# Performance work log

Hardware: AMD Instinct MI355X
Metric: run time of the kernel (lower is better)

Reference implementation:

```python
import jax, jax.numpy as jnp
import numpy as np
from jax import lax

B, T, F, C = 2, 249, 64, 256   # fixed by alpha/beta weight shapes in build()
K = 3                          # conv kernel size
FILT = 256                     # q/k conv filters (both blocks)
V = 256                        # v conv filters (both blocks)
OUT_CH = 64                    # conv2d_final filters (hardcoded)


def conv2d(x, w, b):
    # NHWC 'same' conv, stride 1, dilation 1
    return lax.conv_general_dilated(
        x, w, window_strides=(1, 1), padding='SAME',
        dimension_numbers=('NHWC', 'HWIO', 'NHWC')) + b


def attn_block(x, wq, bq, wk, bk, wv, bv):
    # x: [B, H, L, C]; attention over L per (batch, H) slice
    q = conv2d(x, wq, bq)          # [B,H,L,FILT]
    k = conv2d(x, wk, bk)          # [B,H,L,FILT]
    v = conv2d(x, wv, bv)          # [B,H,L,V]
    scores = jnp.einsum('bhqc,bhkc->bhqk', q, k)   # [B,H,L,L]
    dist = jax.nn.softmax(scores, axis=-1)
    return jnp.einsum('bhqk,bhkc->bhqc', dist, v)  # [B,H,L,V]


def setup_inputs() -> dict:
    key = jax.random.key(0)
    ks = jax.random.split(key, 18)
    s = 0.05
    d = {'x': jax.random.normal(ks[0], (B, T, F, C), jnp.float32)}
    names = ['wq_f', 'wk_f', 'wv_f', 'wq_t', 'wk_t', 'wv_t']
    outs = [FILT, FILT, V, FILT, FILT, V]
    for i, (n, o) in enumerate(zip(names, outs)):
        d[n] = jax.random.normal(ks[1 + i], (K, K, C, o), jnp.float32) * s
        d['b' + n[1:]] = jnp.zeros((o,), jnp.float32)
    d['w_final'] = jax.random.normal(ks[8], (K, K, V + V + C, OUT_CH), jnp.float32) * s
    d['b_final'] = jnp.zeros((OUT_CH,), jnp.float32)
    d['alpha'] = jax.random.uniform(ks[9], (B, T, F, V), jnp.float32, -0.05, 0.05)
    d['beta'] = jax.random.uniform(ks[10], (B, T, F, V), jnp.float32, -0.05, 0.05)
    return d


def reference(x, wq_f, bq_f, wk_f, bk_f, wv_f, bv_f,
              wq_t, bq_t, wk_t, bk_t, wv_t, bv_t,
              w_final, b_final, alpha, beta):
    # AFAB: transpose to [B,F,T,C], attend over time axis T
    xt = jnp.transpose(x, (0, 2, 1, 3))
    out_freq = attn_block(xt, wq_f, bq_f, wk_f, bk_f, wv_f, bv_f)
    out_freq = jnp.transpose(out_freq, (0, 2, 1, 3))  # back to [B,T,F,V]
    # ATAB: attend over frequency axis F directly on [B,T,F,C]
    out_time = attn_block(x, wq_t, bq_t, wk_t, bk_t, wv_t, bv_t)
    # learned elementwise gating + concat + final conv (concatenation=True path)
    fused = jnp.concatenate([alpha * out_freq, beta * out_time, x], axis=-1)
    return conv2d(fused, w_final, b_final)
```

## Files before the change

### kernel.cpp

```cpp
#include <hip/hip_runtime.h>


typedef _Float16 f16;
typedef _Float16 f16x8 __attribute__((ext_vector_type(8)));
typedef float    f32x4 __attribute__((ext_vector_type(4)));

#define B_   2
#define T_   249
#define F_   64
#define TP   251
#define FP   66
#define PIXB (T_*F_)
#define NPIX (B_*PIXB)
#define LPAD 256
#define XPOS (B_*TP*FP)

static constexpr size_t FUSED_BYTES = (size_t)B_*TP*FP*768*2;
static constexpr size_t XPAD_BYTES  = (size_t)B_*TP*FP*256*2;
static constexpr size_t QF_BYTES    = (size_t)B_*64*LPAD*256*2;
static constexpr size_t QT_BYTES    = (size_t)B_*T_*64*256*2;
static constexpr size_t WT_BYTES    = (size_t)9*1536*256*2;
static constexpr size_t WFT_BYTES   = (size_t)9*64*768*2;

static constexpr size_t OFF_FUSED = 0;
static constexpr size_t OFF_XPAD  = OFF_FUSED + FUSED_BYTES;
static constexpr size_t OFF_QF    = OFF_XPAD  + XPAD_BYTES;
static constexpr size_t OFF_KF    = OFF_QF + QF_BYTES;
static constexpr size_t OFF_VF    = OFF_KF + QF_BYTES;
static constexpr size_t OFF_QT    = OFF_VF + QF_BYTES;
static constexpr size_t OFF_KT    = OFF_QT + QT_BYTES;
static constexpr size_t OFF_VT    = OFF_KT + QT_BYTES;
static constexpr size_t OFF_WT    = OFF_VT + QT_BYTES;
static constexpr size_t OFF_WFT   = OFF_WT + WT_BYTES;
static constexpr size_t OFF_BALL  = OFF_WFT + WFT_BYTES;
static constexpr size_t OFF_BF    = OFF_BALL + 1536*4;
static constexpr size_t WS_NEED   = OFF_BF + 64*4;

__device__ __forceinline__ f32x4 mfma16(f16x8 a, f16x8 b, f32x4 c) {
    return __builtin_amdgcn_mfma_f32_16x16x32_f16(a, b, c, 0, 0, 0);
}

__device__ __forceinline__ void gl_lds16(const void* g, void* l) {
    __builtin_amdgcn_global_load_lds(
        (const __attribute__((address_space(1))) unsigned int*)(unsigned long long)g,
        (__attribute__((address_space(3))) unsigned int*)(unsigned int)(unsigned long long)l,
        16, 0, 0);
}

__global__ __launch_bounds__(256) void prep_w(
    const float* __restrict__ wqf, const float* __restrict__ wkf, const float* __restrict__ wvf,
    const float* __restrict__ wqt, const float* __restrict__ wkt, const float* __restrict__ wvt,
    const float* __restrict__ wfin,
    const float* __restrict__ bqf, const float* __restrict__ bkf, const float* __restrict__ bvf,
    const float* __restrict__ bqt, const float* __restrict__ bkt, const float* __restrict__ bvt,
    const float* __restrict__ bfin,
    f16* __restrict__ wT, f16* __restrict__ wfT,
    float* __restrict__ biasAll, float* __restrict__ biasF)
{
    int idx = blockIdx.x*256 + threadIdx.x;
    if (idx < 9*1536*256) {
        int tap = idx / (1536*256);
        int r   = idx - tap*(1536*256);
        int n = r >> 8, c = r & 255;
        int dt = tap/3 - 1, df = tap%3 - 1;
        int blk = n >> 8, nl = n & 255;
        const float* w; int kh, kw;
        if (blk < 3) { w = (blk==0) ? wqf : (blk==1) ? wkf : wvf; kh = df+1; kw = dt+1; }
        else         { w = (blk==3) ? wqt : (blk==4) ? wkt : wvt; kh = dt+1; kw = df+1; }
        wT[idx] = (f16)w[((kh*3 + kw)*256 + c)*256 + nl];
    }
    if (idx < 9*64*768) {
        int tap = idx / (64*768);
        int r   = idx - tap*(64*768);
        int oc = r / 768, cin = r - oc*768;
        int dt = tap/3 - 1, df = tap%3 - 1;
        wfT[idx] = (f16)wfin[(((dt+1)*3 + (df+1))*768 + cin)*64 + oc];
    }
    if (idx < 1536) {
        int blk = idx >> 8, nl = idx & 255;
        const float* bb = (blk==0)?bqf:(blk==1)?bkf:(blk==2)?bvf:(blk==3)?bqt:(blk==4)?bkt:bvt;
        biasAll[idx] = bb[nl];
    }
    if (idx < 64) biasF[idx] = bfin[idx];
}

__global__ __launch_bounds__(256) void prep_x(
    const float* __restrict__ x, f16* __restrict__ xpad, f16* __restrict__ fused)
{
    int tid = blockIdx.x*256 + threadIdx.x;
    int pix = tid >> 5, c8 = (tid & 31)*8;
    int b = pix / PIXB; int r = pix - b*PIXB;
    int t = r >> 6, f = r & 63;
    const float* src = x + (size_t)pix*256 + c8;
    f16x8 v;
#pragma unroll
    for (int j = 0; j < 8; ++j) v[j] = (f16)src[j];
    size_t pp = (size_t)(b*TP + t + 1)*FP + (f + 1);
    *(f16x8*)(xpad + pp*256 + c8) = v;
    *(f16x8*)(fused + pp*768 + 512 + c8) = v;
}

__global__ __launch_bounds__(256) void border_zero(
    f16* __restrict__ xpad, f16* __restrict__ fused)
{
    int pix = blockIdx.x*2 + (threadIdx.x >> 7);
    int tl = threadIdx.x & 127;
    int b = pix / 630; int i = pix - b*630;
    int tp, fp;
    if (i < 66)       { tp = 0;   fp = i; }
    else if (i < 132) { tp = 250; fp = i - 66; }
    else { int j = i - 132; tp = 1 + (j >> 1); fp = (j & 1) * 65; }
    size_t pp = (size_t)(b*TP + tp)*FP + fp;
    f16x8 z = {0, 0, 0, 0, 0, 0, 0, 0};
    if (tl < 32) *(f16x8*)(xpad + pp*256 + tl*8) = z;
    if (tl < 96) *(f16x8*)(fused + pp*768 + tl*8) = z;
}

__global__ __launch_bounds__(512, 2) void conv_qkv(
    const f16* __restrict__ xpad, const f16* __restrict__ wT,
    const float* __restrict__ biasAll,
    f16* __restrict__ qf, f16* __restrict__ kf, f16* __restrict__ vf,
    f16* __restrict__ qt, f16* __restrict__ kt_, f16* __restrict__ vt)
{
    __shared__ f16 smemH[448*64];
    __shared__ f16 smemB[2][256*64];

    const int xcd = blockIdx.x & 7, lin = blockIdx.x >> 3;
    const int mtcnt = (xcd < 6) ? 16 : 15;
    if (lin >= 6*mtcnt) return;
    const int mtbase = (xcd < 6) ? xcd*16 : 96 + (xcd - 6)*15;
    const int nt = lin / mtcnt;
    const int mt = mtbase + (lin - nt*mtcnt);

    const int bb_ = mt / 63;
    const int t0  = (mt - bb_*63) * 4;
    const int Gs66 = (bb_*TP + t0) * 66;

    const int l   = threadIdx.x & 63;
    const int wid = threadIdx.x >> 6;
    const int wm = wid >> 2, wn = wid & 3;

    int hOff[7];
#pragma unroll
    for (int j = 0; j < 7; ++j) {
        int pos = j*64 + wid*8 + (l >> 3);
        int ps = pos;
        if (ps > 395) ps = 395;
        { int pm = XPOS - 1 - (bb_*TP + t0)*66; if (ps > pm) ps = pm; }
        int ch = (l & 7) ^ (ps & 7);
        hOff[j] = (Gs66 + ps)*256 + ch*8;
    }
    int bSrc[4];
#pragma unroll
    for (int j = 0; j < 4; ++j) {
        int row = j*64 + wid*8 + (l >> 3);
        int ch = (l & 7) ^ (row & 7);
        bSrc[j] = (nt*256 + row)*256 + ch*8;
    }

    int pos00[8];
#pragma unroll
    for (int m = 0; m < 8; ++m) {
        int r = wm*128 + m*16 + (l & 15);
        pos00[m] = ((r >> 6) + 1)*66 + (r & 63) + 1;
    }
    int bRow[4], bSw[4];
#pragma unroll
    for (int n = 0; n < 4; ++n) {
        int row = wn*64 + n*16 + (l & 15);
        bRow[n] = row*64; bSw[n] = row & 7;
    }

    f32x4 acc[8][4];
#pragma unroll
    for (int m = 0; m < 8; ++m)
#pragma unroll
        for (int n = 0; n < 4; ++n) acc[m][n] = {0.f, 0.f, 0.f, 0.f};

#define HSTAGE(C) do {                                                         \
        _Pragma("unroll")                                                      \
        for (int j_ = 0; j_ < 7; ++j_)                                         \
            gl_lds16(xpad + hOff[j_] + (C)*64,                                 \
                     smemH + (j_*512 + wid*64)*8);                             \
    } while (0)

#define BSTAGE(TAP, C, NB) do {                                                \
        const f16* wt_ = wT + (size_t)(TAP)*(1536*256) + (C)*64;               \
        _Pragma("unroll")                                                      \
        for (int j_ = 0; j_ < 4; ++j_)                                         \
            gl_lds16(wt_ + bSrc[j_], &smemB[NB][(j_*512 + wid*64)*8]);         \
    } while (0)

#define QCOMP(NB, TAPOFF) do {                                                 \
        int pos_[8];                                                           \
        _Pragma("unroll")                                                      \
        for (int m = 0; m < 8; ++m) pos_[m] = pos00[m] + (TAPOFF);             \
        _Pragma("unroll")                                                      \
        for (int kk = 0; kk < 2; ++kk) {                                       \
            const int cch = kk*4 + (l >> 4);                                   \
            f16x8 af[8], bf[4];                                                \
            _Pragma("unroll")                                                  \
            for (int m = 0; m < 8; ++m)                                        \
                af[m] = *(const f16x8*)(smemH + pos_[m]*64 + ((cch ^ (pos_[m] & 7)) << 3)); \
            _Pragma("unroll")                                                  \
            for (int n = 0; n < 4; ++n)                                        \
                bf[n] = *(const f16x8*)(&smemB[NB][0] + bRow[n] + ((cch ^ bSw[n]) << 3)); \
            __builtin_amdgcn_s_setprio(1);                                     \
            _Pragma("unroll")                                                  \
            for (int m = 0; m < 8; ++m)                                        \
                _Pragma("unroll")                                              \
                for (int n = 0; n < 4; ++n)                                    \
                    acc[m][n] = mfma16(af[m], bf[n], acc[m][n]);               \
            __builtin_amdgcn_s_setprio(0);                                     \
        }                                                                      \
    } while (0)

    int buf = 0;
    HSTAGE(0);
    BSTAGE(0, 0, 0);
    __syncthreads();
    for (int c = 0; c < 4; ++c) {
        for (int tap = 0; tap < 9; ++tap) {
            if (tap < 8)      BSTAGE(tap + 1, c, buf ^ 1);
            else if (c < 3)   BSTAGE(0, c + 1, buf ^ 1);
            const int dt = tap/3 - 1, df = tap - (tap/3)*3 - 1;
            QCOMP(buf, dt*66 + df);
            __syncthreads();
            buf ^= 1;
        }
        if (c < 3) {
            HSTAGE(c + 1);
            __syncthreads();
        }
    }
#undef HSTAGE
#undef BSTAGE
#undef QCOMP

    f16* dst = (nt==0)?qf:(nt==1)?kf:(nt==2)?vf:(nt==3)?qt:(nt==4)?kt_:vt;
#pragma unroll
    for (int m = 0; m < 8; ++m) {
#pragma unroll
        for (int rg = 0; rg < 4; ++rg) {
            int row = wm*128 + m*16 + (l >> 4)*4 + rg;
            int t = t0 + (row >> 6), f = row & 63;
            if (t <= 248) {
#pragma unroll
                for (int n = 0; n < 4; ++n) {
                    int col = wn*64 + n*16 + (l & 15);
                    float v = acc[m][n][rg] + biasAll[nt*256 + col];
                    int off;
                    if (nt < 2)       off = ((bb_*64 + f)*LPAD + t)*256 + col;
                    else if (nt == 2) off = ((bb_*64 + f)*256 + col)*LPAD + t;
                    else if (nt < 5)  off = ((bb_*T_ + t)*64 + f)*256 + col;
                    else              off = ((bb_*T_ + t)*256 + col)*64 + f;
                    dst[off] = (f16)v;
                }
            }
        }
    }
}

__global__ __launch_bounds__(256) void attn_f(
    const f16* __restrict__ qf, const f16* __restrict__ kf, const f16* __restrict__ vf,
    const float* __restrict__ alpha, f16* __restrict__ fused)
{
    __shared__ f16 plds[4][16*256];
    const int l = threadIdx.x & 63;
    const int wid = threadIdx.x >> 6;
    const int head = blockIdx.x >> 2;
    const int qb = blockIdx.x & 3;
    const int b = head >> 6, f = head & 63;
    const f16* qh = qf + (size_t)head*LPAD*256;
    const f16* kh = kf + (size_t)head*LPAD*256;
    const f16* vh = vf + (size_t)head*256*LPAD;
    const int qr0 = qb*64 + wid*16;
    f16* pw = &plds[wid][0];

    f16x8 qa[8];
#pragma unroll
    for (int ks = 0; ks < 8; ++ks)
        qa[ks] = *(const f16x8*)(qh + (qr0 + (l & 15))*256 + ks*32 + (l >> 4)*8);

    f32x4 s[16];
#pragma unroll
    for (int nf = 0; nf < 16; ++nf) s[nf] = {0.f, 0.f, 0.f, 0.f};
#pragma unroll
    for (int ks = 0; ks < 8; ++ks)
#pragma unroll
        for (int nf = 0; nf < 16; ++nf) {
            f16x8 bf = *(const f16x8*)(kh + (nf*16 + (l & 15))*256 + ks*32 + (l >> 4)*8);
            s[nf] = mfma16(qa[ks], bf, s[nf]);
        }

    float inv[4];
#pragma unroll
    for (int rg = 0; rg < 4; ++rg) {
        float m = -1e30f;
#pragma unroll
        for (int nf = 0; nf < 16; ++nf)
            if (nf*16 + (l & 15) < T_) m = fmaxf(m, s[nf][rg]);
#pragma unroll
        for (int d = 1; d < 16; d <<= 1) m = fmaxf(m, __shfl_xor(m, d, 64));
        float sum = 0.f;
#pragma unroll
        for (int nf = 0; nf < 16; ++nf) {
            float p = (nf*16 + (l & 15) < T_) ? __expf(s[nf][rg] - m) : 0.f;
            s[nf][rg] = p;
            sum += p;
        }
#pragma unroll
        for (int d = 1; d < 16; d <<= 1) sum += __shfl_xor(sum, d, 64);
        inv[rg] = 1.f / sum;
    }

#pragma unroll
    for (int nf = 0; nf < 16; ++nf)
#pragma unroll
        for (int rg = 0; rg < 4; ++rg) {
            int row = (l >> 4)*4 + rg;
            int col = nf*16 + (l & 15);
            int byte = (row*512 + col*2) ^ ((row & 7) << 4);
            *(f16*)((char*)pw + byte) = (f16)s[nf][rg];
        }

    f32x4 o[16];
#pragma unroll
    for (int nf = 0; nf < 16; ++nf) o[nf] = {0.f, 0.f, 0.f, 0.f};
#pragma unroll
    for (int ks = 0; ks < 8; ++ks) {
        int row = l & 15;
        int cch = ks*4 + (l >> 4);
        int byte = row*512 + ((cch ^ (row & 7)) << 4);
        f16x8 pa = *(const f16x8*)((const char*)pw + byte);
#pragma unroll
        for (int nf = 0; nf < 16; ++nf) {
            f16x8 bf = *(const f16x8*)(vh + (nf*16 + (l & 15))*LPAD + ks*32 + (l >> 4)*8);
            o[nf] = mfma16(pa, bf, o[nf]);
        }
    }

#pragma unroll
    for (int rg = 0; rg < 4; ++rg) {
        int t = qr0 + (l >> 4)*4 + rg;
        if (t < T_) {
#pragma unroll
            for (int nf = 0; nf < 16; ++nf) {
                int c = nf*16 + (l & 15);
                float v = o[nf][rg] * inv[rg] * alpha[((size_t)(b*T_ + t)*64 + f)*256 + c];
                fused[((size_t)(b*TP + t + 1)*FP + (f + 1))*768 + c] = (f16)v;
            }
        }
    }
}

__global__ __launch_bounds__(256) void attn_t(
    const f16* __restrict__ qt, const f16* __restrict__ kt, const f16* __restrict__ vt,
    const float* __restrict__ beta, f16* __restrict__ fused)
{
    __shared__ f16 plds[4][16*64];
    const int l = threadIdx.x & 63;
    const int wid = threadIdx.x >> 6;
    const int head = blockIdx.x;
    const int b = head / T_, t = head - b*T_;
    const f16* qh = qt + (size_t)head*64*256;
    const f16* kh = kt + (size_t)head*64*256;
    const f16* vh = vt + (size_t)head*256*64;
    const int qr0 = wid*16;
    f16* pw = &plds[wid][0];

    f16x8 qa[8];
#pragma unroll
    for (int ks = 0; ks < 8; ++ks)
        qa[ks] = *(const f16x8*)(qh + (qr0 + (l & 15))*256 + ks*32 + (l >> 4)*8);

    f32x4 s[4];
#pragma unroll
    for (int nf = 0; nf < 4; ++nf) s[nf] = {0.f, 0.f, 0.f, 0.f};
#pragma unroll
    for (int ks = 0; ks < 8; ++ks)
#pragma unroll
        for (int nf = 0; nf < 4; ++nf) {
            f16x8 bf = *(const f16x8*)(kh + (nf*16 + (l & 15))*256 + ks*32 + (l >> 4)*8);
            s[nf] = mfma16(qa[ks], bf, s[nf]);
        }

    float inv[4];
#pragma unroll
    for (int rg = 0; rg < 4; ++rg) {
        float m = -1e30f;
#pragma unroll
        for (int nf = 0; nf < 4; ++nf) m = fmaxf(m, s[nf][rg]);
#pragma unroll
        for (int d = 1; d < 16; d <<= 1) m = fmaxf(m, __shfl_xor(m, d, 64));
        float sum = 0.f;
#pragma unroll
        for (int nf = 0; nf < 4; ++nf) {
            float p = __expf(s[nf][rg] - m);
            s[nf][rg] = p;
            sum += p;
        }
#pragma unroll
        for (int d = 1; d < 16; d <<= 1) sum += __shfl_xor(sum, d, 64);
        inv[rg] = 1.f / sum;
    }

#pragma unroll
    for (int nf = 0; nf < 4; ++nf)
#pragma unroll
        for (int rg = 0; rg < 4; ++rg) {
            int row = (l >> 4)*4 + rg;
            int col = nf*16 + (l & 15);
            int byte = (row*128 + col*2) ^ ((row & 7) << 4);
            *(f16*)((char*)pw + byte) = (f16)s[nf][rg];
        }

    f32x4 o[16];
#pragma unroll
    for (int nf = 0; nf < 16; ++nf) o[nf] = {0.f, 0.f, 0.f, 0.f};
#pragma unroll
    for (int ks = 0; ks < 2; ++ks) {
        int row = l & 15;
        int cch = ks*4 + (l >> 4);
        int byte = row*128 + ((cch ^ (row & 7)) << 4);
        f16x8 pa = *(const f16x8*)((const char*)pw + byte);
#pragma unroll
        for (int nf = 0; nf < 16; ++nf) {
            f16x8 bf = *(const f16x8*)(vh + (nf*16 + (l & 15))*64 + ks*32 + (l >> 4)*8);
            o[nf] = mfma16(pa, bf, o[nf]);
        }
    }

#pragma unroll
    for (int rg = 0; rg < 4; ++rg) {
        int fo = qr0 + (l >> 4)*4 + rg;
#pragma unroll
        for (int nf = 0; nf < 16; ++nf) {
            int c = nf*16 + (l & 15);
            float v = o[nf][rg] * inv[rg] * beta[((size_t)(b*T_ + t)*64 + fo)*256 + c];
            fused[((size_t)(b*TP + t + 1)*FP + (fo + 1))*768 + 256 + c] = (f16)v;
        }
    }
}

__global__ __launch_bounds__(256, 2) void conv_final(
    const f16* __restrict__ fused, const f16* __restrict__ wfT,
    const float* __restrict__ biasF, float* __restrict__ out)
{
    __shared__ f16 smemH[288*64];
    __shared__ f16 smemB[2][64*64];

    const int mt = blockIdx.x;
    const int bb = mt / 125;
    const int t0 = (mt - bb*125) * 2;
    const int Gs66 = (bb*TP + t0) * 66;

    const int tid = threadIdx.x;
    const int l   = tid & 63;
    const int wid = tid >> 6;
    const int wm = wid >> 1, wn = wid & 1;

    int hOff[9];
#pragma unroll
    for (int j = 0; j < 9; ++j) {
        int ps = j*32 + (tid >> 3);
        if (ps > 263) ps = 263;
        { int pm = XPOS - 1 - (bb*TP + t0)*66; if (ps > pm) ps = pm; }
        int ch = (tid & 7) ^ (ps & 7);
        hOff[j] = (Gs66 + ps)*768 + ch*8;
    }
    int bSrc[2];
#pragma unroll
    for (int j = 0; j < 2; ++j) {
        int row = j*32 + (tid >> 3);
        int ch  = (tid & 7) ^ (row & 7);
        bSrc[j] = row*768 + ch*8;
    }

    int pos00[4];
#pragma unroll
    for (int m = 0; m < 4; ++m) {
        int r = wm*64 + m*16 + (l & 15);
        pos00[m] = ((r >> 6) + 1)*66 + (r & 63) + 1;
    }
    int bRow[2], bSw[2];
#pragma unroll
    for (int n = 0; n < 2; ++n) {
        int row = wn*32 + n*16 + (l & 15);
        bRow[n] = row*64; bSw[n] = row & 7;
    }

    f32x4 acc[4][2];
#pragma unroll
    for (int m = 0; m < 4; ++m)
#pragma unroll
        for (int n = 0; n < 2; ++n) acc[m][n] = {0.f, 0.f, 0.f, 0.f};

#define FHSTAGE(C) do {                                                        \
        _Pragma("unroll")                                                      \
        for (int j_ = 0; j_ < 9; ++j_)                                         \
            gl_lds16(fused + hOff[j_] + (C)*64,                                \
                     smemH + (j_*256 + wid*64)*8);                             \
    } while (0)

#define FBSTAGE(TAP, C, NB) do {                                               \
        const f16* wt_ = wfT + (size_t)(TAP)*(64*768) + (C)*64;                \
        _Pragma("unroll")                                                      \
        for (int j_ = 0; j_ < 2; ++j_)                                         \
            gl_lds16(wt_ + bSrc[j_], &smemB[NB][(j_*256 + wid*64)*8]);         \
    } while (0)

#define FCOMP(NB, TAPOFF) do {                                                 \
        int pos_[4];                                                           \
        _Pragma("unroll")                                                      \
        for (int m = 0; m < 4; ++m) pos_[m] = pos00[m] + (TAPOFF);             \
        _Pragma("unroll")                                                      \
        for (int kk = 0; kk < 2; ++kk) {                                       \
            const int cch = kk*4 + (l >> 4);                                   \
            f16x8 af[4], bf[2];                                                \
            _Pragma("unroll")                                                  \
            for (int m = 0; m < 4; ++m)                                        \
                af[m] = *(const f16x8*)(smemH + pos_[m]*64 + ((cch ^ (pos_[m] & 7)) << 3)); \
            _Pragma("unroll")                                                  \
            for (int n = 0; n < 2; ++n)                                        \
                bf[n] = *(const f16x8*)(&smemB[NB][0] + bRow[n] + ((cch ^ bSw[n]) << 3)); \
            __builtin_amdgcn_s_setprio(1);                                     \
            _Pragma("unroll")                                                  \
            for (int m = 0; m < 4; ++m)                                        \
                _Pragma("unroll")                                              \
                for (int n = 0; n < 2; ++n)                                    \
                    acc[m][n] = mfma16(af[m], bf[n], acc[m][n]);               \
            __builtin_amdgcn_s_setprio(0);                                     \
        }                                                                      \
    } while (0)

    int buf = 0;
    FHSTAGE(0);
    FBSTAGE(0, 0, 0);
    __syncthreads();
    for (int c = 0; c < 12; ++c) {
        for (int tap = 0; tap < 9; ++tap) {
            if (tap < 8)       FBSTAGE(tap + 1, c, buf ^ 1);
            else if (c < 11)   FBSTAGE(0, c + 1, buf ^ 1);
            const int dt = tap/3 - 1, df = tap - (tap/3)*3 - 1;
            FCOMP(buf, dt*66 + df);
            __syncthreads();
            buf ^= 1;
        }
        if (c < 11) {
            FHSTAGE(c + 1);
            __syncthreads();
        }
    }
#undef FHSTAGE
#undef FBSTAGE
#undef FCOMP

#pragma unroll
    for (int m = 0; m < 4; ++m) {
#pragma unroll
        for (int rg = 0; rg < 4; ++rg) {
            int r = wm*64 + m*16 + (l >> 4)*4 + rg;
            int t = t0 + (r >> 6), f = r & 63;
            if (t <= 248) {
                size_t pix = (size_t)bb*PIXB + t*64 + f;
#pragma unroll
                for (int n = 0; n < 2; ++n) {
                    int oc = wn*32 + n*16 + (l & 15);
                    out[pix*64 + oc] = acc[m][n][rg] + biasF[oc];
                }
            }
        }
    }
}

extern "C" void kernel_launch(void* const* d_in, const int* in_sizes, int n_in,
                              void* d_out, int out_size, void* d_ws, size_t ws_size,
                              hipStream_t stream) {
    (void)in_sizes; (void)n_in; (void)out_size;
    const float* x    = (const float*)d_in[0];
    const float* wqf  = (const float*)d_in[1];
    const float* bqf  = (const float*)d_in[2];
    const float* wkf  = (const float*)d_in[3];
    const float* bkf  = (const float*)d_in[4];
    const float* wvf  = (const float*)d_in[5];
    const float* bvf  = (const float*)d_in[6];
    const float* wqt  = (const float*)d_in[7];
    const float* bqt  = (const float*)d_in[8];
    const float* wkt  = (const float*)d_in[9];
    const float* bkt  = (const float*)d_in[10];
    const float* wvt  = (const float*)d_in[11];
    const float* bvt  = (const float*)d_in[12];
    const float* wfin = (const float*)d_in[13];
    const float* bfin = (const float*)d_in[14];
    const float* alpha= (const float*)d_in[15];
    const float* beta = (const float*)d_in[16];

    if (ws_size < WS_NEED) return;

    char* ws = (char*)d_ws;
    f16* fused  = (f16*)(ws + OFF_FUSED);
    f16* xpad   = (f16*)(ws + OFF_XPAD);
    f16* qf     = (f16*)(ws + OFF_QF);
    f16* kf     = (f16*)(ws + OFF_KF);
    f16* vf     = (f16*)(ws + OFF_VF);
    f16* qt     = (f16*)(ws + OFF_QT);
    f16* kt     = (f16*)(ws + OFF_KT);
    f16* vt     = (f16*)(ws + OFF_VT);
    f16* wT     = (f16*)(ws + OFF_WT);
    f16* wfT    = (f16*)(ws + OFF_WFT);
    float* bAll = (float*)(ws + OFF_BALL);
    float* bF   = (float*)(ws + OFF_BF);

    hipMemsetAsync(vf, 0, QF_BYTES, stream);

    border_zero<<<dim3(630), dim3(256), 0, stream>>>(xpad, fused);
    prep_w<<<dim3((9*1536*256 + 255)/256), dim3(256), 0, stream>>>(
        wqf, wkf, wvf, wqt, wkt, wvt, wfin,
        bqf, bkf, bvf, bqt, bkt, bvt, bfin, wT, wfT, bAll, bF);
    prep_x<<<dim3(NPIX*32/256), dim3(256), 0, stream>>>(x, xpad, fused);
    conv_qkv<<<dim3(768), dim3(512), 0, stream>>>(xpad, wT, bAll, qf, kf, vf, qt, kt, vt);
    attn_f<<<dim3(512), dim3(256), 0, stream>>>(qf, kf, vf, alpha, fused);
    attn_t<<<dim3(498), dim3(256), 0, stream>>>(qt, kt, vt, beta, fused);
    conv_final<<<dim3(250), dim3(256), 0, stream>>>(fused, wfT, bF, (float*)d_out);
}
```

Measured before the change: 502.2 us.

## Restructure QKV conv into 192-row tiles with triple-buffered A and interleaved loads

The implicit-GEMM QKV conv changes from 256-pixel M-tiles (4 time rows, with a halo tile staged once per channel chunk) to 192-pixel tiles of 3 exact time rows. A is now loaded per tap and channel chunk into a triple-buffered LDS ring, and B is double-buffered. Global-to-LDS loads are interleaved between MFMA sub-steps, with explicit vmcnt waits and sched barriers, to overlap memory with compute and remove the padded rows past T. Dropping the halo reuse means more global A traffic, the grid grows to 1008 blocks, and the occupancy hint on launch bounds is removed.

```diff
diff --git a/kernel.cpp b/kernel.cpp
--- a/kernel.cpp
+++ b/kernel.cpp
@@ -116,146 +116,187 @@
     if (tl < 96) *(f16x8*)(fused + pp*768 + tl*8) = z;
 }
 
-__global__ __launch_bounds__(512, 2) void conv_qkv(
+__global__ __launch_bounds__(512) void conv_qkv(
     const f16* __restrict__ xpad, const f16* __restrict__ wT,
     const float* __restrict__ biasAll,
     f16* __restrict__ qf, f16* __restrict__ kf, f16* __restrict__ vf,
     f16* __restrict__ qt, f16* __restrict__ kt_, f16* __restrict__ vt)
 {
-    __shared__ f16 smemH[448*64];
-    __shared__ f16 smemB[2][256*64];
+    __shared__ f16 smemA[3*12288];
+    __shared__ f16 smemB[2*16384];
 
     const int xcd = blockIdx.x & 7, lin = blockIdx.x >> 3;
-    const int mtcnt = (xcd < 6) ? 16 : 15;
+    const int mtcnt = (xcd < 6) ? 21 : 20;
     if (lin >= 6*mtcnt) return;
-    const int mtbase = (xcd < 6) ? xcd*16 : 96 + (xcd - 6)*15;
-    const int nt = lin / mtcnt;
-    const int mt = mtbase + (lin - nt*mtcnt);
-
-    const int bb_ = mt / 63;
-    const int t0  = (mt - bb_*63) * 4;
-    const int Gs66 = (bb_*TP + t0) * 66;
+    const int mtbase = (xcd < 6) ? xcd*21 : 126 + (xcd - 6)*20;
+    int nt, mi;
+    if (xcd < 6) { nt = lin / 21; mi = lin - nt*21; }
+    else         { nt = lin / 20; mi = lin - nt*20; }
+    const int mt = mtbase + mi;
+
+    const int bb = mt / 83;
+    const int t0 = (mt - bb*83) * 3;
 
     const int l   = threadIdx.x & 63;
     const int wid = threadIdx.x >> 6;
     const int wm = wid >> 2, wn = wid & 3;
 
-    int hOff[7];
-#pragma unroll
-    for (int j = 0; j < 7; ++j) {
-        int pos = j*64 + wid*8 + (l >> 3);
-        int ps = pos;
-        if (ps > 395) ps = 395;
-        { int pm = XPOS - 1 - (bb_*TP + t0)*66; if (ps > pm) ps = pm; }
-        int ch = (l & 7) ^ (ps & 7);
-        hOff[j] = (Gs66 + ps)*256 + ch*8;
-    }
-    int bSrc[4];
-#pragma unroll
-    for (int j = 0; j < 4; ++j) {
-        int row = j*64 + wid*8 + (l >> 3);
-        int ch = (l & 7) ^ (row & 7);
-        bSrc[j] = (nt*256 + row)*256 + ch*8;
-    }
-
-    int pos00[8];
-#pragma unroll
-    for (int m = 0; m < 8; ++m) {
-        int r = wm*128 + m*16 + (l & 15);
-        pos00[m] = ((r >> 6) + 1)*66 + (r & 63) + 1;
-    }
-    int bRow[4], bSw[4];
+    int aS[3];
+#pragma unroll
+    for (int u = 0; u < 3; ++u) {
+        int r = u*64 + wid*8 + (l >> 3);
+        int t = t0 + (r >> 6), f = r & 63;
+        int ch = (l & 7) ^ (r & 7);
+        aS[u] = ((bb*TP + t + 1)*FP + (f + 1))*256 + ch*8;
+    }
+    int bS[4];
+#pragma unroll
+    for (int u = 0; u < 4; ++u) {
+        int r = u*64 + wid*8 + (l >> 3);
+        int ch = (l & 7) ^ (r & 7);
+        bS[u] = (nt*256 + r)*256 + ch*8;
+    }
+
+    int aOff[6], aKey[6];
+#pragma unroll
+    for (int m = 0; m < 6; ++m) {
+        int lr = wm*96 + m*16 + (l & 15);
+        aOff[m] = lr*64; aKey[m] = lr & 7;
+    }
+    int bOff[4], bKey[4];
 #pragma unroll
     for (int n = 0; n < 4; ++n) {
-        int row = wn*64 + n*16 + (l & 15);
-        bRow[n] = row*64; bSw[n] = row & 7;
-    }
-
-    f32x4 acc[8][4];
-#pragma unroll
-    for (int m = 0; m < 8; ++m)
+        int lr = wn*64 + n*16 + (l & 15);
+        bOff[n] = lr*64; bKey[n] = lr & 7;
+    }
+
+    f32x4 acc[6][4];
+#pragma unroll
+    for (int m = 0; m < 6; ++m)
 #pragma unroll
         for (int n = 0; n < 4; ++n) acc[m][n] = {0.f, 0.f, 0.f, 0.f};
 
-#define HSTAGE(C) do {                                                         \
+#define SB  __builtin_amdgcn_sched_barrier(0)
+#define BARRIER do { SB; __builtin_amdgcn_s_barrier(); SB; } while (0)
+#define READ_A(DST, S, KK, BASE) do {                                          \
+        const int cch_ = (KK)*4 + (l >> 4);                                    \
         _Pragma("unroll")                                                      \
-        for (int j_ = 0; j_ < 7; ++j_)                                         \
-            gl_lds16(xpad + hOff[j_] + (C)*64,                                 \
-                     smemH + (j_*512 + wid*64)*8);                             \
+        for (int m_ = 0; m_ < 3; ++m_)                                         \
+            DST[m_] = *(const f16x8*)((BASE) + aOff[(S)*3 + m_]                \
+                                      + ((cch_ ^ aKey[(S)*3 + m_]) << 3));     \
     } while (0)
-
-#define BSTAGE(TAP, C, NB) do {                                                \
-        const f16* wt_ = wT + (size_t)(TAP)*(1536*256) + (C)*64;               \
+#define READ_B(KK, BASE) do {                                                  \
+        const int cch_ = (KK)*4 + (l >> 4);                                    \
         _Pragma("unroll")                                                      \
-        for (int j_ = 0; j_ < 4; ++j_)                                         \
-            gl_lds16(wt_ + bSrc[j_], &smemB[NB][(j_*512 + wid*64)*8]);         \
+        for (int n_ = 0; n_ < 4; ++n_)                                         \
+            bf[n_] = *(const f16x8*)((BASE) + bOff[n_]                         \
+                                     + ((cch_ ^ bKey[n_]) << 3));              \
     } while (0)
-
-#define QCOMP(NB, TAPOFF) do {                                                 \
-        int pos_[8];                                                           \
+#define MFMA12(AF, S) do {                                                     \
+        __builtin_amdgcn_s_setprio(1);                                         \
         _Pragma("unroll")                                                      \
-        for (int m = 0; m < 8; ++m) pos_[m] = pos00[m] + (TAPOFF);             \
-        _Pragma("unroll")                                                      \
-        for (int kk = 0; kk < 2; ++kk) {                                       \
-            const int cch = kk*4 + (l >> 4);                                   \
-            f16x8 af[8], bf[4];                                                \
+        for (int m_ = 0; m_ < 3; ++m_)                                         \
             _Pragma("unroll")                                                  \
-            for (int m = 0; m < 8; ++m)                                        \
-                af[m] = *(const f16x8*)(smemH + pos_[m]*64 + ((cch ^ (pos_[m] & 7)) << 3)); \
-            _Pragma("unroll")                                                  \
-            for (int n = 0; n < 4; ++n)                                        \
-                bf[n] = *(const f16x8*)(&smemB[NB][0] + bRow[n] + ((cch ^ bSw[n]) << 3)); \
-            __builtin_amdgcn_s_setprio(1);                                     \
-            _Pragma("unroll")                                                  \
-            for (int m = 0; m < 8; ++m)                                        \
-                _Pragma("unroll")                                              \
-                for (int n = 0; n < 4; ++n)                                    \
-                    acc[m][n] = mfma16(af[m], bf[n], acc[m][n]);               \
-            __builtin_amdgcn_s_setprio(0);                                     \
-        }                                                                      \
+            for (int n_ = 0; n_ < 4; ++n_)                                     \
+                acc[(S)*3 + m_][n_] = mfma16(AF[m_], bf[n_], acc[(S)*3 + m_][n_]); \
+        __builtin_amdgcn_s_setprio(0);                                         \
     } while (0)
 
-    int buf = 0;
-    HSTAGE(0);
-    BSTAGE(0, 0, 0);
-    __syncthreads();
-    for (int c = 0; c < 4; ++c) {
-        for (int tap = 0; tap < 9; ++tap) {
-            if (tap < 8)      BSTAGE(tap + 1, c, buf ^ 1);
-            else if (c < 3)   BSTAGE(0, c + 1, buf ^ 1);
-            const int dt = tap/3 - 1, df = tap - (tap/3)*3 - 1;
-            QCOMP(buf, dt*66 + df);
-            __syncthreads();
-            buf ^= 1;
-        }
-        if (c < 3) {
-            HSTAGE(c + 1);
-            __syncthreads();
-        }
-    }
-#undef HSTAGE
-#undef BSTAGE
-#undef QCOMP
+    {
+        const int ash0 = ((0/3 - 1)*FP + (0%3 - 1))*256;
+#pragma unroll
+        for (int u = 0; u < 3; ++u)
+            gl_lds16(xpad + aS[u] + ash0, smemA + (u*64 + wid*8)*64);
+#pragma unroll
+        for (int u = 0; u < 4; ++u)
+            gl_lds16(wT + bS[u], smemB + (u*64 + wid*8)*64);
+        const int ash1 = ash0 + 64;
+#pragma unroll
+        for (int u = 0; u < 3; ++u)
+            gl_lds16(xpad + aS[u] + ash1, smemA + 12288 + (u*64 + wid*8)*64);
+        SB;
+        asm volatile("s_waitcnt vmcnt(3)" ::: "memory");
+        __builtin_amdgcn_s_barrier();
+        SB;
+    }
+
+#pragma unroll 1
+    for (int kt = 0; kt < 36; ++kt) {
+        const int a  = kt - (kt/3)*3;
+        const int aN = (kt+2) - ((kt+2)/3)*3;
+        const int d  = kt & 1;
+        const f16* Ac = smemA + a*12288;
+        const f16* Bc = smemB + d*16384;
+        f16* An = smemA + aN*12288;
+        f16* Bn = smemB + (d ^ 1)*16384;
+        const bool doB = (kt + 1) < 36, doA = (kt + 2) < 36;
+        int ktB = kt + 1, ktA = kt + 2;
+        int tapB = ktB >> 2, kcB = ktB & 3;
+        size_t bshB = (size_t)tapB*(1536*256) + kcB*64;
+        int tapA = ktA >> 2, kcA = ktA & 3;
+        int ashA = ((tapA/3 - 1)*FP + (tapA%3 - 1))*256 + kcA*64;
+
+        f16x8 bf[4], af0[3], af1[3];
+
+        READ_B(0, Bc);
+        READ_A(af0, 0, 0, Ac);
+        if (doB) {
+            gl_lds16(wT + bS[0] + bshB, Bn + (0*64 + wid*8)*64);
+            gl_lds16(wT + bS[1] + bshB, Bn + (1*64 + wid*8)*64);
+        }
+        BARRIER;
+        MFMA12(af0, 0);
+
+        READ_A(af1, 1, 0, Ac);
+        if (doB) {
+            gl_lds16(wT + bS[2] + bshB, Bn + (2*64 + wid*8)*64);
+            gl_lds16(wT + bS[3] + bshB, Bn + (3*64 + wid*8)*64);
+        }
+        BARRIER;
+        MFMA12(af1, 1);
+
+        READ_B(1, Bc);
+        READ_A(af0, 0, 1, Ac);
+        if (doA) {
+            gl_lds16(xpad + aS[0] + ashA, An + (0*64 + wid*8)*64);
+            gl_lds16(xpad + aS[1] + ashA, An + (1*64 + wid*8)*64);
+        }
+        BARRIER;
+        MFMA12(af0, 0);
+
+        READ_A(af1, 1, 1, Ac);
+        if (doA)
+            gl_lds16(xpad + aS[2] + ashA, An + (2*64 + wid*8)*64);
+        SB;
+        if (kt < 34) asm volatile("s_waitcnt vmcnt(3)" ::: "memory");
+        else         asm volatile("s_waitcnt vmcnt(0)" ::: "memory");
+        __builtin_amdgcn_s_barrier();
+        SB;
+        MFMA12(af1, 1);
+    }
+#undef SB
+#undef BARRIER
+#undef READ_A
+#undef READ_B
+#undef MFMA12
 
     f16* dst = (nt==0)?qf:(nt==1)?kf:(nt==2)?vf:(nt==3)?qt:(nt==4)?kt_:vt;
 #pragma unroll
-    for (int m = 0; m < 8; ++m) {
+    for (int m = 0; m < 6; ++m) {
 #pragma unroll
         for (int rg = 0; rg < 4; ++rg) {
-            int row = wm*128 + m*16 + (l >> 4)*4 + rg;
+            int row = wm*96 + m*16 + (l >> 4)*4 + rg;
             int t = t0 + (row >> 6), f = row & 63;
-            if (t <= 248) {
-#pragma unroll
-                for (int n = 0; n < 4; ++n) {
-                    int col = wn*64 + n*16 + (l & 15);
-                    float v = acc[m][n][rg] + biasAll[nt*256 + col];
-                    int off;
-                    if (nt < 2)       off = ((bb_*64 + f)*LPAD + t)*256 + col;
-                    else if (nt == 2) off = ((bb_*64 + f)*256 + col)*LPAD + t;
-                    else if (nt < 5)  off = ((bb_*T_ + t)*64 + f)*256 + col;
-                    else              off = ((bb_*T_ + t)*256 + col)*64 + f;
-                    dst[off] = (f16)v;
-                }
+#pragma unroll
+            for (int n = 0; n < 4; ++n) {
+                int col = wn*64 + n*16 + (l & 15);
+                float v = acc[m][n][rg] + biasAll[nt*256 + col];
+                int off;
+                if (nt < 2)       off = ((bb*64 + f)*LPAD + t)*256 + col;
+                else if (nt == 2) off = ((bb*64 + f)*256 + col)*LPAD + t;
+                else if (nt < 5)  off = ((bb*T_ + t)*64 + f)*256 + col;
+                else              off = ((bb*T_ + t)*256 + col)*64 + f;
+                dst[off] = (f16)v;
             }
         }
     }
@@ -619,7 +660,7 @@
         wqf, wkf, wvf, wqt, wkt, wvt, wfin,
         bqf, bkf, bvf, bqt, bkt, bvt, bfin, wT, wfT, bAll, bF);
     prep_x<<<dim3(NPIX*32/256), dim3(256), 0, stream>>>(x, xpad, fused);
-    conv_qkv<<<dim3(768), dim3(512), 0, stream>>>(xpad, wT, bAll, qf, kf, vf, qt, kt, vt);
+    conv_qkv<<<dim3(1008), dim3(512), 0, stream>>>(xpad, wT, bAll, qf, kf, vf, qt, kt, vt);
     attn_f<<<dim3(512), dim3(256), 0, stream>>>(qf, kf, vf, alpha, fused);
     attn_t<<<dim3(498), dim3(256), 0, stream>>>(qt, kt, vt, beta, fused);
     conv_final<<<dim3(250), dim3(256), 0, stream>>>(fused, wfT, bF, (float*)d_out);
```

Result: faster. 486.1 us (-3.2%).
